# Performance work log

Hardware: AMD Instinct MI355X
Metric: run time of the kernel (lower is better)

The kernel has to match this reference:

```python
import jax, jax.numpy as jnp
import numpy as np

DEPTH, B, S, E, H, EXP = 6, 16, 511, 1024, 16, 2
HD = E // H
FF = EXP * E


def _layernorm(x, g, b, eps=1e-5):
    m = jnp.mean(x, axis=-1, keepdims=True)
    v = jnp.var(x, axis=-1, keepdims=True)
    return (x - m) * jax.lax.rsqrt(v + eps) * g + b


def setup_inputs() -> dict:
    key = jax.random.key(0)
    ks = jax.random.split(key, 12)
    sc = 0.02
    inp = {
        "x": jax.random.normal(ks[0], (B, S, E), jnp.float32),
        "cls_token": jax.random.normal(ks[1], (1, 1, E), jnp.float32),
        "pos_emb": jax.random.normal(ks[2], (1, S + 1, E), jnp.float32),
        # attention projections (bias=False in source), stacked over depth
        "Wq": jax.random.normal(ks[3], (DEPTH, E, E), jnp.float32) * sc,
        "Wk": jax.random.normal(ks[4], (DEPTH, E, E), jnp.float32) * sc,
        "Wv": jax.random.normal(ks[5], (DEPTH, E, E), jnp.float32) * sc,
        "Wp": jax.random.normal(ks[6], (DEPTH, E, E), jnp.float32) * sc,
        # layernorm params
        "ln1_g": jnp.ones((DEPTH, E), jnp.float32),
        "ln1_b": jnp.zeros((DEPTH, E), jnp.float32),
        "ln2_g": jnp.ones((DEPTH, E), jnp.float32),
        "ln2_b": jnp.zeros((DEPTH, E), jnp.float32),
        # feed-forward (with bias, as nn.Linear default)
        "W1": jax.random.normal(ks[7], (DEPTH, E, FF), jnp.float32) * sc,
        "b1": jnp.zeros((DEPTH, FF), jnp.float32),
        "W2": jax.random.normal(ks[8], (DEPTH, FF, E), jnp.float32) * sc,
        "b2": jnp.zeros((DEPTH, E), jnp.float32),
    }
    return inp


def reference(x, cls_token, pos_emb, Wq, Wk, Wv, Wp,
              ln1_g, ln1_b, ln2_g, ln2_b, W1, b1, W2, b2):
    b = x.shape[0]
    # AddClsToken + PositionalEmbedding
    h = jnp.concatenate([jnp.broadcast_to(cls_token, (b, 1, E)), x], axis=1) + pos_emb
    scale = jnp.asarray(E ** 0.5, h.dtype)  # source scales by sqrt(emb_size)
    for i in range(DEPTH):
        # --- self-attention sublayer (pre-LN) ---
        res = h
        xn = _layernorm(h, ln1_g[i], ln1_b[i])
        q = (xn @ Wq[i]).reshape(b, -1, H, HD).transpose(0, 2, 1, 3)  # b h n d
        k = (xn @ Wk[i]).reshape(b, -1, H, HD).transpose(0, 2, 1, 3)
        v = (xn @ Wv[i]).reshape(b, -1, H, HD).transpose(0, 2, 1, 3)
        energy = jnp.einsum('bhqd,bhkd->bhqk', q, k)
        att = jax.nn.softmax(energy / scale, axis=-1)
        out = jnp.einsum('bhqk,bhkd->bhqd', att, v)
        out = out.transpose(0, 2, 1, 3).reshape(b, -1, E)
        h = out @ Wp[i] + res
        # --- feed-forward sublayer (pre-LN) ---
        res = h
        yn = _layernorm(h, ln2_g[i], ln2_b[i])
        ff = jax.nn.gelu(yn @ W1[i] + b1[i], approximate=False) @ W2[i] + b2[i]
        h = ff + res
    return h
```

## Files before the change

### kernel.cpp

```cpp
#include <hip/hip_runtime.h>
#include <cstdint>
#include <cstddef>

#define DEPTH 6
#define NB    16
#define NSEQ  512
#define EMB   1024
#define NHEAD 16
#define HDIM  64
#define FFD   2048
#define NTOK  (NB * NSEQ)

typedef unsigned short u16;
using bf16x8 = __attribute__((ext_vector_type(8))) __bf16;
using f32x4  = __attribute__((ext_vector_type(4))) float;
using u16x4  = __attribute__((ext_vector_type(4))) u16;

typedef __attribute__((address_space(1))) uint32_t* as1_u32p;
typedef __attribute__((address_space(3))) uint32_t* as3_u32p;
typedef __attribute__((address_space(3))) u16*      as3_u16p;

__device__ __forceinline__ u16 f2bf(float f) {
  union { float f; uint32_t u; } v; v.f = f;
  uint32_t u = v.u;
  return (u16)((u + 0x7FFFu + ((u >> 16) & 1u)) >> 16);
}

__device__ __forceinline__ void gload_lds16(const u16* g, u16* l) {
  void* gp = const_cast<u16*>(g);
  __builtin_amdgcn_global_load_lds((as1_u32p)gp, (as3_u32p)l, 16, 0, 0);
}

template<int ROWBYTES>
__device__ __forceinline__ void stage16k(const u16* g0, int ldk, u16* lds) {
  int t = threadIdx.x;
#pragma unroll
  for (int i = 0; i < 4; ++i) {
    int off = (i * 256 + t) * 16;
    int row = off / ROWBYTES;
    int pc  = (off % ROWBYTES) >> 4;
    int lc  = pc ^ (row & 7);
    gload_lds16(g0 + (size_t)row * ldk + lc * 8, lds + (off >> 1));
  }
}

__global__ __launch_bounds__(256)
void wprep_k(const float* __restrict__ W, u16* __restrict__ Wt,
             int K, int N, size_t inL, size_t outL, size_t outOff)
{
  int ntiles = N >> 6, ktiles = K >> 6;
  int bid = blockIdx.x;
  int l = bid / (ktiles * ntiles);
  int r = bid % (ktiles * ntiles);
  int kt = r / ntiles, nt = r % ntiles;
  const float* in = W + (size_t)l * inL + (size_t)(kt * 64) * N + nt * 64;
  u16* out = Wt + (size_t)l * outL + outOff + (size_t)(nt * 64) * K + kt * 64;
  __shared__ float tile[64][65];
  int t = threadIdx.x;
  int tr = t >> 4, tc = (t & 15) * 4;
#pragma unroll
  for (int i = 0; i < 4; ++i) {
    f32x4 v = *(const f32x4*)(in + (size_t)(tr + i * 16) * N + tc);
    tile[tr + i * 16][tc + 0] = v[0];
    tile[tr + i * 16][tc + 1] = v[1];
    tile[tr + i * 16][tc + 2] = v[2];
    tile[tr + i * 16][tc + 3] = v[3];
  }
  __syncthreads();
#pragma unroll
  for (int i = 0; i < 4; ++i) {
    int nr = tr + i * 16;
    u16x4 o;
    o[0] = f2bf(tile[tc + 0][nr]);
    o[1] = f2bf(tile[tc + 1][nr]);
    o[2] = f2bf(tile[tc + 2][nr]);
    o[3] = f2bf(tile[tc + 3][nr]);
    *(u16x4*)(out + (size_t)nr * K + tc) = o;
  }
}

__global__ __launch_bounds__(256)
void embed_k(const float* __restrict__ x, const float* __restrict__ cls,
             const float* __restrict__ pos, float* __restrict__ H)
{
  int row = blockIdx.x, t = threadIdx.x;
  int b_ = row >> 9, n = row & 511;
  int c = t * 4;
  f32x4 p = *(const f32x4*)(pos + (size_t)n * EMB + c);
  f32x4 s;
  if (n == 0) s = *(const f32x4*)(cls + c);
  else        s = *(const f32x4*)(x + ((size_t)b_ * 511 + (n - 1)) * EMB + c);
  f32x4 o = s + p;
  *(f32x4*)(H + (size_t)row * EMB + c) = o;
}

__global__ __launch_bounds__(256)
void ln_k(const float* __restrict__ H, const float* __restrict__ g,
          const float* __restrict__ b, u16* __restrict__ out)
{
  int row = blockIdx.x, t = threadIdx.x;
  const float* hp = H + (size_t)row * EMB;
  f32x4 v = *(const f32x4*)(hp + t * 4);
  float s  = v[0] + v[1] + v[2] + v[3];
  float ss = v[0]*v[0] + v[1]*v[1] + v[2]*v[2] + v[3]*v[3];
#pragma unroll
  for (int m = 1; m <= 32; m <<= 1) { s += __shfl_xor(s, m); ss += __shfl_xor(ss, m); }
  __shared__ float red[8];
  if ((t & 63) == 0) { red[(t >> 6) * 2] = s; red[(t >> 6) * 2 + 1] = ss; }
  __syncthreads();
  float S  = red[0] + red[2] + red[4] + red[6];
  float SS = red[1] + red[3] + red[5] + red[7];
  float mean = S * (1.0f / EMB);
  float var  = SS * (1.0f / EMB) - mean * mean;
  float rs = rsqrtf(var + 1e-5f);
  f32x4 gg = *(const f32x4*)(g + t * 4);
  f32x4 bb = *(const f32x4*)(b + t * 4);
  u16x4 o;
#pragma unroll
  for (int i = 0; i < 4; ++i) o[i] = f2bf((v[i] - mean) * rs * gg[i] + bb[i]);
  *(u16x4*)(out + (size_t)row * EMB + t * 4) = o;
}


__device__ __forceinline__ void stageA256(u16* dst, const u16* src, int K,
                                          int half, int t) {
#pragma unroll
  for (int i = 0; i < 2; ++i) {
    int off = (i * 512 + t) * 16;
    int chunk = off >> 13;
    int row_in = (off >> 7) & 63;
    int lc = ((off >> 4) & 7) ^ (row_in & 7);
    int grow = chunk * 128 + half * 64 + row_in;
    gload_lds16(src + (size_t)grow * K + lc * 8, dst + (off >> 1));
  }
}

__device__ __forceinline__ void stageB256(u16* dst, const u16* src, int K,
                                          int half, int t) {
#pragma unroll
  for (int i = 0; i < 2; ++i) {
    int off = (i * 512 + t) * 16;
    int blk = off >> 12;
    int row_in = (off >> 7) & 31;
    int lc = ((off >> 4) & 7) ^ (row_in & 7);
    int nrow = blk * 64 + half * 32 + row_in;
    gload_lds16(src + (size_t)nrow * K + lc * 8, dst + (off >> 1));
  }
}

#define DS_A(BUF, MH) do {                                                   \
  const char* _ba = (const char*)&smA[BUF][MH][wm][0];                       \
  _Pragma("unroll") for (int mf = 0; mf < 4; ++mf) {                         \
    int ri = mf * 16 + r0; int swz = (r0 & 7) << 4;                          \
    af[mf][0] = *(const bf16x8*)(_ba + ri * 128 + ((kk0 * 2) ^ swz));        \
    af[mf][1] = *(const bf16x8*)(_ba + ri * 128 + (((32 + kk0) * 2) ^ swz)); \
  } } while (0)

#define DS_B(BUF, NH) do {                                                   \
  const char* _bb = (const char*)&smB[BUF][NH][wn][0];                       \
  _Pragma("unroll") for (int nf = 0; nf < 2; ++nf) {                         \
    int ri = nf * 16 + r0; int swz = (r0 & 7) << 4;                          \
    bfr[nf][0] = *(const bf16x8*)(_bb + ri * 128 + ((kk0 * 2) ^ swz));       \
    bfr[nf][1] = *(const bf16x8*)(_bb + ri * 128 + (((32 + kk0) * 2) ^ swz));\
  } } while (0)

#define MFMA16(MH, NH) do {                                                  \
  __builtin_amdgcn_s_setprio(1);                                             \
  _Pragma("unroll") for (int ks = 0; ks < 2; ++ks)                           \
  _Pragma("unroll") for (int mf = 0; mf < 4; ++mf)                           \
  _Pragma("unroll") for (int nf = 0; nf < 2; ++nf)                           \
    acc[MH * 4 + mf][NH * 2 + nf] = __builtin_amdgcn_mfma_f32_16x16x32_bf16( \
        af[mf][ks], bfr[nf][ks], acc[MH * 4 + mf][NH * 2 + nf], 0, 0, 0);    \
  __builtin_amdgcn_s_setprio(0);                                             \
} while (0)

#define BAR()       __builtin_amdgcn_s_barrier()
#define WAIT_LGKM0() do { asm volatile("s_waitcnt lgkmcnt(0)" ::: "memory"); \
                          __builtin_amdgcn_sched_barrier(0); } while (0)
#define VMCNT4()    asm volatile("s_waitcnt vmcnt(4)" ::: "memory")

template<int EPI>
__global__ __launch_bounds__(512, 2)
void gemm256_k(const u16* __restrict__ A, const u16* __restrict__ Bt,
               int nbn, int K,
               const float* __restrict__ bias, u16* __restrict__ outB,
               u16* __restrict__ qo, u16* __restrict__ ko, u16* __restrict__ vto)
{
  __shared__ u16 smA[2][2][2][4096];
  __shared__ u16 smB[2][2][4][2048];

  int cpx = gridDim.x >> 3;
  int logical = (blockIdx.x & 7) * cpx + (blockIdx.x >> 3);
  int bm = logical / nbn, bn = logical % nbn;
  int t = threadIdx.x, lane = t & 63, w = t >> 6;
  int wm = w >> 2, wn = w & 3;
  int r0 = lane & 15, hi = lane >> 4, kk0 = hi * 8;
  const u16* Ab = A  + (size_t)(bm * 256) * K;
  const u16* Bb = Bt + (size_t)(bn * 256) * K;
  int nkt = K >> 6, T = nkt >> 1;

  stageA256(&smA[0][0][0][0], Ab, K, 0, t);
  stageA256(&smA[0][1][0][0], Ab, K, 1, t);
  stageB256(&smB[0][0][0][0], Bb, K, 0, t);
  stageB256(&smB[0][1][0][0], Bb, K, 1, t);
  stageA256(&smA[1][0][0][0], Ab + 64, K, 0, t);
  stageB256(&smB[1][1][0][0], Bb + 64, K, 1, t);
  VMCNT4();
  BAR();

  const f32x4 vzero = {0.f, 0.f, 0.f, 0.f};
  f32x4 acc[8][4];
#pragma unroll
  for (int i = 0; i < 8; ++i)
#pragma unroll
    for (int j = 0; j < 4; ++j) acc[i][j] = vzero;

  bf16x8 af[4][2], bfr[2][2];

  for (int it = 0; it < T; ++it) {
    int k1 = 2 * it + 1;
    int k2 = 2 * it + 2; if (k2 > nkt - 1) k2 = nkt - 1;
    int k3 = 2 * it + 3; if (k3 > nkt - 1) k3 = nkt - 1;
    DS_A(0, 0); DS_B(0, 0);
    stageA256(&smA[1][1][0][0], Ab + k1 * 64, K, 1, t);
    BAR(); WAIT_LGKM0(); MFMA16(0, 0); BAR();
    DS_B(0, 1);
    stageB256(&smB[1][0][0][0], Bb + k1 * 64, K, 0, t);
    BAR(); WAIT_LGKM0(); MFMA16(0, 1); BAR();
    DS_A(0, 1);
    stageA256(&smA[0][0][0][0], Ab + k2 * 64, K, 0, t);
    BAR(); WAIT_LGKM0(); MFMA16(1, 1); BAR();
    DS_B(0, 0);
    stageB256(&smB[0][1][0][0], Bb + k2 * 64, K, 1, t);
    VMCNT4();
    BAR(); WAIT_LGKM0(); MFMA16(1, 0); BAR();
    DS_A(1, 0); DS_B(1, 0);
    stageA256(&smA[0][1][0][0], Ab + k2 * 64, K, 1, t);
    BAR(); WAIT_LGKM0(); MFMA16(0, 0); BAR();
    DS_B(1, 1);
    stageB256(&smB[0][0][0][0], Bb + k2 * 64, K, 0, t);
    BAR(); WAIT_LGKM0(); MFMA16(0, 1); BAR();
    DS_A(1, 1);
    stageA256(&smA[1][0][0][0], Ab + k3 * 64, K, 0, t);
    BAR(); WAIT_LGKM0(); MFMA16(1, 1); BAR();
    DS_B(1, 0);
    stageB256(&smB[1][1][0][0], Bb + k3 * 64, K, 1, t);
    VMCNT4();
    BAR(); WAIT_LGKM0(); MFMA16(1, 0); BAR();
  }

  int m0 = bm * 256 + wm * 128;
  int n0 = bn * 256 + wn * 64;
#pragma unroll
  for (int mi = 0; mi < 8; ++mi) {
#pragma unroll
    for (int ni = 0; ni < 4; ++ni) {
      int col  = n0 + ni * 16 + r0;
      int rowb = m0 + mi * 16 + hi * 4;
      if (EPI == 0) {
        int which = col >> 10, c = col & 1023;
        int hh = c >> 6, d = c & 63;
        int b_ = rowb >> 9, n_ = rowb & 511;
        size_t bh = (size_t)(b_ * NHEAD + hh);
        if (which == 2) {
          u16x4 o;
#pragma unroll
          for (int j = 0; j < 4; ++j) o[j] = f2bf(acc[mi][ni][j]);
          *(u16x4*)(vto + (bh * HDIM + d) * NSEQ + n_) = o;
        } else {
          u16* dst = (which == 0) ? qo : ko;
#pragma unroll
          for (int j = 0; j < 4; ++j)
            dst[(bh * NSEQ + n_ + j) * HDIM + d] = f2bf(acc[mi][ni][j]);
        }
      } else {
#pragma unroll
        for (int j = 0; j < 4; ++j) {
          float xg = acc[mi][ni][j] + bias[col];
          float ge = 0.5f * xg * (1.0f + erff(xg * 0.70710678118654752f));
          outB[(size_t)(rowb + j) * FFD + col] = f2bf(ge);
        }
      }
    }
  }
}

template<int EPI>
__global__ __launch_bounds__(256, 2)
void gemm_k(const u16* __restrict__ A, const u16* __restrict__ Bt,
            int nbn, int K,
            const float* __restrict__ bias, float* __restrict__ H)
{
  __shared__ u16 sm[2][2][128 * 64];
  int cpx = gridDim.x >> 3;
  int logical = (blockIdx.x & 7) * cpx + (blockIdx.x >> 3);
  int bm = logical / nbn, bn = logical % nbn;
  int t = threadIdx.x, lane = t & 63, w = t >> 6;
  int wm = w >> 1, wn = w & 1;
  const u16* Ab = A  + (size_t)(bm * 128) * K;
  const u16* Bb = Bt + (size_t)(bn * 128) * K;
  int nkt = K >> 6;

  stage16k<128>(Ab, K, &sm[0][0][0]);
  stage16k<128>(Bb, K, &sm[0][1][0]);
  __syncthreads();

  const f32x4 vzero = {0.f, 0.f, 0.f, 0.f};
  f32x4 acc[4][4];
#pragma unroll
  for (int i = 0; i < 4; ++i)
#pragma unroll
    for (int j = 0; j < 4; ++j) acc[i][j] = vzero;

  int r0 = lane & 15;
  int kk0 = (lane >> 4) * 8;

  for (int kt = 0; kt < nkt; ++kt) {
    int cur = kt & 1;
    if (kt + 1 < nkt) {
      stage16k<128>(Ab + (kt + 1) * 64, K, &sm[cur ^ 1][0][0]);
      stage16k<128>(Bb + (kt + 1) * 64, K, &sm[cur ^ 1][1][0]);
    }
    const char* smAp = (const char*)&sm[cur][0][0];
    const char* smBp = (const char*)&sm[cur][1][0];
#pragma unroll
    for (int ks = 0; ks < 2; ++ks) {
      int kk = ks * 32 + kk0;
      bf16x8 a[4], b[4];
#pragma unroll
      for (int mf = 0; mf < 4; ++mf) {
        int row = wm * 64 + mf * 16 + r0;
        a[mf] = *(const bf16x8*)(smAp + row * 128 + ((kk * 2) ^ ((row & 7) << 4)));
      }
#pragma unroll
      for (int nf = 0; nf < 4; ++nf) {
        int row = wn * 64 + nf * 16 + r0;
        b[nf] = *(const bf16x8*)(smBp + row * 128 + ((kk * 2) ^ ((row & 7) << 4)));
      }
#pragma unroll
      for (int mf = 0; mf < 4; ++mf)
#pragma unroll
        for (int nf = 0; nf < 4; ++nf)
          acc[mf][nf] = __builtin_amdgcn_mfma_f32_16x16x32_bf16(a[mf], b[nf], acc[mf][nf], 0, 0, 0);
    }
    __syncthreads();
  }

  int m0 = bm * 128 + wm * 64;
  int n0 = bn * 128 + wn * 64;
  int hi = lane >> 4;
#pragma unroll
  for (int mf = 0; mf < 4; ++mf) {
#pragma unroll
    for (int nf = 0; nf < 4; ++nf) {
      int col  = n0 + nf * 16 + r0;
      int rowb = m0 + mf * 16 + hi * 4;
#pragma unroll
      for (int j = 0; j < 4; ++j) {
        int row = rowb + j;
        float v = acc[mf][nf][j];
        size_t idx = (size_t)row * EMB + col;
        if (EPI == 1) H[idx] = v + H[idx];
        else          H[idx] = v + bias[col] + H[idx];
      }
    }
  }
}

__global__ __launch_bounds__(256, 3)
void attn_k(const u16* __restrict__ Q, const u16* __restrict__ Kk,
            const u16* __restrict__ Vt, u16* __restrict__ AO)
{
  __shared__ u16 kv[2][8192];
  __shared__ u16 Pt[4][2048];
  int bid = blockIdx.x;
  int bh = (bid & 7) * 32 + (bid >> 6);
  int qt = (bid >> 3) & 7;
  int t = threadIdx.x, lane = t & 63, w = t >> 6;
  const u16* Kb = Kk + (size_t)bh * (NSEQ * HDIM);
  const u16* Vb = Vt + (size_t)bh * (HDIM * NSEQ);
  int r0 = lane & 15, hi = lane >> 4, kk0 = hi * 8;

  int qrow = qt * 64 + w * 16 + r0;
  const u16* Qp = Q + ((size_t)bh * NSEQ + qrow) * HDIM;
  bf16x8 qf0 = *(const bf16x8*)(Qp + kk0);
  bf16x8 qf1 = *(const bf16x8*)(Qp + 32 + kk0);

  const f32x4 vzero = {0.f, 0.f, 0.f, 0.f};
  f32x4 accS[32];
#pragma unroll
  for (int f = 0; f < 32; ++f) accS[f] = vzero;

  stage16k<128>(Kb, HDIM, &kv[0][0]);
  __syncthreads();
#pragma unroll
  for (int kt = 0; kt < 4; ++kt) {
    if (kt < 3) stage16k<128>(Kb + (size_t)(kt + 1) * 128 * HDIM, HDIM, &kv[(kt + 1) & 1][0]);
    const char* smK = (const char*)&kv[kt & 1][0];
#pragma unroll
    for (int nfl = 0; nfl < 8; ++nfl) {
      int krow = nfl * 16 + r0;
      int swz = (krow & 7) << 4;
      bf16x8 b0 = *(const bf16x8*)(smK + krow * 128 + (((kk0)      * 2) ^ swz));
      bf16x8 b1 = *(const bf16x8*)(smK + krow * 128 + (((32 + kk0) * 2) ^ swz));
      accS[kt * 8 + nfl] = __builtin_amdgcn_mfma_f32_16x16x32_bf16(qf0, b0, accS[kt * 8 + nfl], 0, 0, 0);
      accS[kt * 8 + nfl] = __builtin_amdgcn_mfma_f32_16x16x32_bf16(qf1, b1, accS[kt * 8 + nfl], 0, 0, 0);
    }
    __syncthreads();
  }

  stage16k<256>(Vb, NSEQ, &kv[0][0]);

  float mx[4], den[4], rden[4];
#pragma unroll
  for (int j = 0; j < 4; ++j) {
    float m = -1e30f;
#pragma unroll
    for (int f = 0; f < 32; ++f) m = fmaxf(m, accS[f][j]);
    m = fmaxf(m, __shfl_xor(m, 1));
    m = fmaxf(m, __shfl_xor(m, 2));
    m = fmaxf(m, __shfl_xor(m, 4));
    m = fmaxf(m, __shfl_xor(m, 8));
    mx[j] = m;
    den[j] = 0.f;
  }
  uint32_t pb[64];
#pragma unroll
  for (int f = 0; f < 32; ++f) {
    float p0 = __expf((accS[f][0] - mx[0]) * 0.03125f);
    float p1 = __expf((accS[f][1] - mx[1]) * 0.03125f);
    float p2 = __expf((accS[f][2] - mx[2]) * 0.03125f);
    float p3 = __expf((accS[f][3] - mx[3]) * 0.03125f);
    den[0] += p0; den[1] += p1; den[2] += p2; den[3] += p3;
    pb[f * 2 + 0] = (uint32_t)f2bf(p0) | ((uint32_t)f2bf(p1) << 16);
    pb[f * 2 + 1] = (uint32_t)f2bf(p2) | ((uint32_t)f2bf(p3) << 16);
  }
#pragma unroll
  for (int j = 0; j < 4; ++j) {
    float d = den[j];
    d += __shfl_xor(d, 1); d += __shfl_xor(d, 2);
    d += __shfl_xor(d, 4); d += __shfl_xor(d, 8);
    rden[j] = 1.0f / d;
  }
  __syncthreads();

  int perm0 = ((r0 & 4) << 2) + ((r0 >> 3) << 2) + (r0 & 3);
  uint32_t ptb = (uint32_t)(uintptr_t)(as3_u16p)&Pt[w][0];
  uint32_t trBase = ptb + r0 * 2 + hi * 128;
  char* PtW = (char*)&Pt[w][0];

  f32x4 accO[4];
#pragma unroll
  for (int nf = 0; nf < 4; ++nf) accO[nf] = vzero;

#pragma unroll
  for (int kt = 0; kt < 4; ++kt) {
    if (kt < 3) stage16k<256>(Vb + (kt + 1) * 128, NSEQ, &kv[(kt + 1) & 1][0]);
#pragma unroll
    for (int fl = 0; fl < 8; ++fl) {
      int f = kt * 8 + fl;
      int row = (fl >> 1) * 32 + perm0 + ((fl & 1) << 3);
      *(uint2*)(PtW + row * 32 + hi * 8) = make_uint2(pb[f * 2], pb[f * 2 + 1]);
    }
    asm volatile("s_waitcnt lgkmcnt(0)" ::: "memory");
    const char* smV = (const char*)&kv[kt & 1][0];
#pragma unroll
    for (int s = 0; s < 4; ++s) {
      uint2 t0, t1;
      uint32_t a0 = trBase + s * 1024;
      asm volatile("ds_read_b64_tr_b16 %0, %1" : "=v"(t0) : "v"(a0) : "memory");
      asm volatile("ds_read_b64_tr_b16 %0, %1" : "=v"(t1) : "v"(a0 + 512) : "memory");
      bf16x8 vb[4];
#pragma unroll
      for (int nf = 0; nf < 4; ++nf) {
        int d = nf * 16 + r0;
        int inrow = s * 64 + hi * 16;
        vb[nf] = *(const bf16x8*)(smV + d * 256 + (inrow ^ ((d & 7) << 4)));
      }
      asm volatile("s_waitcnt lgkmcnt(0)" ::: "memory");
      __builtin_amdgcn_sched_barrier(0);
      union { uint4 u; bf16x8 v; } pa;
      pa.u = make_uint4(t0.x, t0.y, t1.x, t1.y);
#pragma unroll
      for (int nf = 0; nf < 4; ++nf)
        accO[nf] = __builtin_amdgcn_mfma_f32_16x16x32_bf16(pa.v, vb[nf], accO[nf], 0, 0, 0);
    }
    __syncthreads();
  }

  int b_ = bh >> 4, hh = bh & 15;
#pragma unroll
  for (int nf = 0; nf < 4; ++nf)
#pragma unroll
    for (int j = 0; j < 4; ++j) {
      int ql = hi * 4 + j;
      int tok = qt * 64 + w * 16 + ql;
      int col = hh * 64 + nf * 16 + r0;
      AO[((size_t)(b_ * NSEQ + tok)) * EMB + col] = f2bf(accO[nf][j] * rden[j]);
    }
}

extern "C" void kernel_launch(void* const* d_in, const int* in_sizes, int n_in,
                              void* d_out, int out_size, void* d_ws, size_t ws_size,
                              hipStream_t stream)
{
  const float* x    = (const float*)d_in[0];
  const float* cls  = (const float*)d_in[1];
  const float* pos  = (const float*)d_in[2];
  const float* Wq   = (const float*)d_in[3];
  const float* Wk   = (const float*)d_in[4];
  const float* Wv   = (const float*)d_in[5];
  const float* Wp   = (const float*)d_in[6];
  const float* ln1g = (const float*)d_in[7];
  const float* ln1b = (const float*)d_in[8];
  const float* ln2g = (const float*)d_in[9];
  const float* ln2b = (const float*)d_in[10];
  const float* W1   = (const float*)d_in[11];
  const float* b1   = (const float*)d_in[12];
  const float* W2   = (const float*)d_in[13];
  const float* b2   = (const float*)d_in[14];
  float* H = (float*)d_out;

  char* ws = (char*)d_ws;
  u16* wqkv = (u16*)(ws + 0);
  u16* wp   = (u16*)(ws + 37748736);
  u16* w1t  = (u16*)(ws + 50331648);
  u16* w2t  = (u16*)(ws + 75497472);
  u16* xn   = (u16*)(ws + 100663296);
  u16* qb   = (u16*)(ws + 117440512);
  u16* kb   = (u16*)(ws + 134217728);
  u16* vtb  = (u16*)(ws + 150994944);
  u16* ffb  = qb;

  wprep_k<<<1536, 256, 0, stream>>>(Wq, wqkv, 1024, 1024, 1048576, 3145728, 0);
  wprep_k<<<1536, 256, 0, stream>>>(Wk, wqkv, 1024, 1024, 1048576, 3145728, 1048576);
  wprep_k<<<1536, 256, 0, stream>>>(Wv, wqkv, 1024, 1024, 1048576, 3145728, 2097152);
  wprep_k<<<1536, 256, 0, stream>>>(Wp, wp,   1024, 1024, 1048576, 1048576, 0);
  wprep_k<<<3072, 256, 0, stream>>>(W1, w1t,  1024, 2048, 2097152, 2097152, 0);
  wprep_k<<<3072, 256, 0, stream>>>(W2, w2t,  2048, 1024, 2097152, 2097152, 0);

  embed_k<<<NTOK, 256, 0, stream>>>(x, cls, pos, H);

  for (int l = 0; l < DEPTH; ++l) {
    ln_k<<<NTOK, 256, 0, stream>>>(H, ln1g + l * EMB, ln1b + l * EMB, xn);
    gemm256_k<0><<<384, 512, 0, stream>>>(xn, wqkv + (size_t)l * 3145728, 12, 1024,
                                          nullptr, nullptr, qb, kb, vtb);
    attn_k<<<2048, 256, 0, stream>>>(qb, kb, vtb, xn);
    gemm_k<1><<<512, 256, 0, stream>>>(xn, wp + (size_t)l * 1048576, 8, 1024,
                                       nullptr, H);
    ln_k<<<NTOK, 256, 0, stream>>>(H, ln2g + l * EMB, ln2b + l * EMB, xn);
    gemm256_k<2><<<256, 512, 0, stream>>>(xn, w1t + (size_t)l * 2097152, 8, 1024,
                                          b1 + l * FFD, ffb, nullptr, nullptr, nullptr);
    gemm_k<3><<<512, 256, 0, stream>>>(ffb, w2t + (size_t)l * 2097152, 8, 2048,
                                       b2 + l * EMB, H);
  }
}
```

Baseline: 1.613 ms.

## Double-buffer MFMA fragment registers to overlap LDS reads with matrix math

Restructures the 256x256 GEMM main loop so the A and B register fragments are double-buffered (afA/afB, bfX/bfY). The next sub-tile's LDS reads are issued before the current MFMA block, with partial lgkmcnt waits in place of full drains. This also drops one barrier per phase and reorders the global-to-LDS staging schedule, adding a full prologue load. The goal is to hide LDS latency and barrier stalls behind MFMA work, at the cost of extra VGPR pressure under the 2-waves-per-SIMD launch bound and a trickier correctness argument for buffer reuse.

```diff
diff --git a/kernel.cpp b/kernel.cpp
--- a/kernel.cpp
+++ b/kernel.cpp
@@ -122,62 +122,58 @@
 }
 
 
-__device__ __forceinline__ void stageA256(u16* dst, const u16* src, int K,
-                                          int half, int t) {
+__device__ __forceinline__ void stageA256(u16* dst, const u16* src, int K, int t) {
 #pragma unroll
   for (int i = 0; i < 2; ++i) {
     int off = (i * 512 + t) * 16;
     int chunk = off >> 13;
     int row_in = (off >> 7) & 63;
     int lc = ((off >> 4) & 7) ^ (row_in & 7);
-    int grow = chunk * 128 + half * 64 + row_in;
-    gload_lds16(src + (size_t)grow * K + lc * 8, dst + (off >> 1));
-  }
-}
-
-__device__ __forceinline__ void stageB256(u16* dst, const u16* src, int K,
-                                          int half, int t) {
+    gload_lds16(src + (size_t)(chunk * 128 + row_in) * K + lc * 8, dst + (off >> 1));
+  }
+}
+
+__device__ __forceinline__ void stageB256(u16* dst, const u16* src, int K, int t) {
 #pragma unroll
   for (int i = 0; i < 2; ++i) {
     int off = (i * 512 + t) * 16;
     int blk = off >> 12;
     int row_in = (off >> 7) & 31;
     int lc = ((off >> 4) & 7) ^ (row_in & 7);
-    int nrow = blk * 64 + half * 32 + row_in;
-    gload_lds16(src + (size_t)nrow * K + lc * 8, dst + (off >> 1));
-  }
-}
-
-#define DS_A(BUF, MH) do {                                                   \
+    gload_lds16(src + (size_t)(blk * 64 + row_in) * K + lc * 8, dst + (off >> 1));
+  }
+}
+
+#define RD_A(SET, BUF, MH) do {                                              \
   const char* _ba = (const char*)&smA[BUF][MH][wm][0];                       \
   _Pragma("unroll") for (int mf = 0; mf < 4; ++mf) {                         \
-    int ri = mf * 16 + r0; int swz = (r0 & 7) << 4;                          \
-    af[mf][0] = *(const bf16x8*)(_ba + ri * 128 + ((kk0 * 2) ^ swz));        \
-    af[mf][1] = *(const bf16x8*)(_ba + ri * 128 + (((32 + kk0) * 2) ^ swz)); \
+    int ri = mf * 16 + r0;                                                   \
+    SET[mf][0] = *(const bf16x8*)(_ba + ri * 128 + ((kk0 * 2) ^ swz));       \
+    SET[mf][1] = *(const bf16x8*)(_ba + ri * 128 + (((32 + kk0) * 2) ^ swz));\
   } } while (0)
 
-#define DS_B(BUF, NH) do {                                                   \
+#define RD_B(SET, BUF, NH) do {                                              \
   const char* _bb = (const char*)&smB[BUF][NH][wn][0];                       \
   _Pragma("unroll") for (int nf = 0; nf < 2; ++nf) {                         \
-    int ri = nf * 16 + r0; int swz = (r0 & 7) << 4;                          \
-    bfr[nf][0] = *(const bf16x8*)(_bb + ri * 128 + ((kk0 * 2) ^ swz));       \
-    bfr[nf][1] = *(const bf16x8*)(_bb + ri * 128 + (((32 + kk0) * 2) ^ swz));\
+    int ri = nf * 16 + r0;                                                   \
+    SET[nf][0] = *(const bf16x8*)(_bb + ri * 128 + ((kk0 * 2) ^ swz));       \
+    SET[nf][1] = *(const bf16x8*)(_bb + ri * 128 + (((32 + kk0) * 2) ^ swz));\
   } } while (0)
 
-#define MFMA16(MH, NH) do {                                                  \
+#define MM(SA, SB, MH, NH) do {                                              \
   __builtin_amdgcn_s_setprio(1);                                             \
   _Pragma("unroll") for (int ks = 0; ks < 2; ++ks)                           \
   _Pragma("unroll") for (int mf = 0; mf < 4; ++mf)                           \
   _Pragma("unroll") for (int nf = 0; nf < 2; ++nf)                           \
     acc[MH * 4 + mf][NH * 2 + nf] = __builtin_amdgcn_mfma_f32_16x16x32_bf16( \
-        af[mf][ks], bfr[nf][ks], acc[MH * 4 + mf][NH * 2 + nf], 0, 0, 0);    \
+        SA[mf][ks], SB[nf][ks], acc[MH * 4 + mf][NH * 2 + nf], 0, 0, 0);     \
   __builtin_amdgcn_s_setprio(0);                                             \
 } while (0)
 
-#define BAR()       __builtin_amdgcn_s_barrier()
-#define WAIT_LGKM0() do { asm volatile("s_waitcnt lgkmcnt(0)" ::: "memory"); \
-                          __builtin_amdgcn_sched_barrier(0); } while (0)
-#define VMCNT4()    asm volatile("s_waitcnt vmcnt(4)" ::: "memory")
+#define BARR()   asm volatile("s_barrier" ::: "memory")
+#define WAITC(N) do { asm volatile("s_waitcnt lgkmcnt(" #N ")" ::: "memory"); \
+                      __builtin_amdgcn_sched_barrier(0); } while (0)
+#define VM4()    asm volatile("s_waitcnt vmcnt(4)" ::: "memory")
 
 template<int EPI>
 __global__ __launch_bounds__(512, 2)
@@ -195,18 +191,21 @@
   int t = threadIdx.x, lane = t & 63, w = t >> 6;
   int wm = w >> 2, wn = w & 3;
   int r0 = lane & 15, hi = lane >> 4, kk0 = hi * 8;
+  int swz = (r0 & 7) << 4;
   const u16* Ab = A  + (size_t)(bm * 256) * K;
   const u16* Bb = Bt + (size_t)(bn * 256) * K;
   int nkt = K >> 6, T = nkt >> 1;
 
-  stageA256(&smA[0][0][0][0], Ab, K, 0, t);
-  stageA256(&smA[0][1][0][0], Ab, K, 1, t);
-  stageB256(&smB[0][0][0][0], Bb, K, 0, t);
-  stageB256(&smB[0][1][0][0], Bb, K, 1, t);
-  stageA256(&smA[1][0][0][0], Ab + 64, K, 0, t);
-  stageB256(&smB[1][1][0][0], Bb + 64, K, 1, t);
-  VMCNT4();
-  BAR();
+  stageA256(&smA[0][0][0][0], Ab + 0 * 64 + 0 * 64 * K, K, t);
+  stageB256(&smB[0][0][0][0], Bb + 0 * 64 + 0 * 32 * K, K, t);
+  stageB256(&smB[0][1][0][0], Bb + 0 * 64 + 32 * K, K, t);
+  stageA256(&smA[0][1][0][0], Ab + 0 * 64 + 64 * K, K, t);
+  stageA256(&smA[1][0][0][0], Ab + 1 * 64, K, t);
+  stageB256(&smB[1][0][0][0], Bb + 1 * 64, K, t);
+  stageB256(&smB[1][1][0][0], Bb + 1 * 64 + 32 * K, K, t);
+  stageA256(&smA[1][1][0][0], Ab + 1 * 64 + 64 * K, K, t);
+  asm volatile("s_waitcnt vmcnt(0)" ::: "memory");
+  BARR();
 
   const f32x4 vzero = {0.f, 0.f, 0.f, 0.f};
   f32x4 acc[8][4];
@@ -215,39 +214,41 @@
 #pragma unroll
     for (int j = 0; j < 4; ++j) acc[i][j] = vzero;
 
-  bf16x8 af[4][2], bfr[2][2];
+  bf16x8 afA[4][2], afB[4][2], bfX[2][2], bfY[2][2];
+  RD_A(afA, 0, 0);
+  RD_B(bfX, 0, 0);
 
   for (int it = 0; it < T; ++it) {
-    int k1 = 2 * it + 1;
-    int k2 = 2 * it + 2; if (k2 > nkt - 1) k2 = nkt - 1;
-    int k3 = 2 * it + 3; if (k3 > nkt - 1) k3 = nkt - 1;
-    DS_A(0, 0); DS_B(0, 0);
-    stageA256(&smA[1][1][0][0], Ab + k1 * 64, K, 1, t);
-    BAR(); WAIT_LGKM0(); MFMA16(0, 0); BAR();
-    DS_B(0, 1);
-    stageB256(&smB[1][0][0][0], Bb + k1 * 64, K, 0, t);
-    BAR(); WAIT_LGKM0(); MFMA16(0, 1); BAR();
-    DS_A(0, 1);
-    stageA256(&smA[0][0][0][0], Ab + k2 * 64, K, 0, t);
-    BAR(); WAIT_LGKM0(); MFMA16(1, 1); BAR();
-    DS_B(0, 0);
-    stageB256(&smB[0][1][0][0], Bb + k2 * 64, K, 1, t);
-    VMCNT4();
-    BAR(); WAIT_LGKM0(); MFMA16(1, 0); BAR();
-    DS_A(1, 0); DS_B(1, 0);
-    stageA256(&smA[0][1][0][0], Ab + k2 * 64, K, 1, t);
-    BAR(); WAIT_LGKM0(); MFMA16(0, 0); BAR();
-    DS_B(1, 1);
-    stageB256(&smB[0][0][0][0], Bb + k2 * 64, K, 0, t);
-    BAR(); WAIT_LGKM0(); MFMA16(0, 1); BAR();
-    DS_A(1, 1);
-    stageA256(&smA[1][0][0][0], Ab + k3 * 64, K, 0, t);
-    BAR(); WAIT_LGKM0(); MFMA16(1, 1); BAR();
-    DS_B(1, 0);
-    stageB256(&smB[1][1][0][0], Bb + k3 * 64, K, 1, t);
-    VMCNT4();
-    BAR(); WAIT_LGKM0(); MFMA16(1, 0); BAR();
-  }
+    int k2 = 2 * it + 2; if (k2 >= nkt) k2 = nkt - 1;
+    int k3 = 2 * it + 3; if (k3 >= nkt) k3 = nkt - 1;
+    RD_B(bfY, 0, 1);
+    stageA256(&smA[0][0][0][0], Ab + k2 * 64 + 0 * K, K, t);
+    WAITC(4); MM(afA, bfX, 0, 0); BARR();
+    RD_A(afB, 0, 1);
+    stageB256(&smB[0][0][0][0], Bb + k2 * 64 + 0 * K, K, t);
+    WAITC(8); MM(afA, bfY, 0, 1); BARR();
+    RD_A(afA, 1, 0);
+    stageB256(&smB[0][1][0][0], Bb + k2 * 64 + 32 * K, K, t);
+    WAITC(8); MM(afB, bfY, 1, 1); BARR();
+    RD_B(bfY, 1, 0);
+    stageA256(&smA[0][1][0][0], Ab + k2 * 64 + 64 * K, K, t);
+    VM4();
+    WAITC(4); MM(afB, bfX, 1, 0); BARR();
+    RD_B(bfX, 1, 1);
+    stageA256(&smA[1][0][0][0], Ab + k3 * 64 + 0 * K, K, t);
+    WAITC(4); MM(afA, bfY, 0, 0); BARR();
+    RD_A(afB, 1, 1);
+    stageB256(&smB[1][0][0][0], Bb + k3 * 64 + 0 * K, K, t);
+    WAITC(8); MM(afA, bfX, 0, 1); BARR();
+    RD_A(afA, 0, 0);
+    stageB256(&smB[1][1][0][0], Bb + k3 * 64 + 32 * K, K, t);
+    WAITC(8); MM(afB, bfX, 1, 1); BARR();
+    RD_B(bfX, 0, 0);
+    stageA256(&smA[1][1][0][0], Ab + k3 * 64 + 64 * K, K, t);
+    VM4();
+    WAITC(4); MM(afB, bfY, 1, 0); BARR();
+  }
+  asm volatile("s_waitcnt vmcnt(0)" ::: "memory");
 
   int m0 = bm * 256 + wm * 128;
   int n0 = bn * 256 + wn * 64;
```

Measured after the change: 1.571 ms. 2.6% less time.
